# Kernel tuning notes

Measured on AMD Instinct MI355X. Metric: run time of the kernel, lower is better.

## Reference

```python
import jax, jax.numpy as jnp
import numpy as np

MLP_DIMS = [256, 128, 64, 32, 1]

def setup_inputs() -> dict:
    key = jax.random.key(0)
    ks = jax.random.split(key, 16)
    N, C, sp = 2, 256, 512
    inp = {
        'points': jax.random.normal(ks[0], (N, C, sp), dtype=jnp.float32),
        'heatMap': jax.random.uniform(ks[1], (N, sp, sp), dtype=jnp.float32),
        'mask': jnp.ones((N, sp, sp), dtype=jnp.float32),
        'positiveMask': jax.random.uniform(ks[2], (N, sp, sp), dtype=jnp.float32),
    }
    # MLP params: 256->128->64->32->1, Kaiming-ish scale
    for i, (din, dout) in enumerate(zip(MLP_DIMS[:-1], MLP_DIMS[1:])):
        inp[f'W{i}'] = jax.random.normal(ks[4 + i], (din, dout), dtype=jnp.float32) * (1.0 / np.sqrt(din))
        inp[f'b{i}'] = jnp.zeros((dout,), dtype=jnp.float32)
    return inp


def _mlp(x, Ws, bs):
    # Linear+ReLU cascade; final layer is a raw logit (no activation).
    n = len(Ws)
    for i, (W, b) in enumerate(zip(Ws, bs)):
        x = jnp.einsum('...i,io->...o', x, W) + b
        if i < n - 1:
            x = jax.nn.relu(x)
    return x


def _bce_with_logits(logits, targets):
    # stable elementwise BCE-with-logits, reduction='none'
    return jnp.maximum(logits, 0.0) - logits * targets + jnp.log1p(jnp.exp(-jnp.abs(logits)))


def reference(points, heatMap, mask, positiveMask, W0, b0, W1, b1, W2, b2, W3, b3):
    p = jnp.transpose(points, (0, 2, 1))          # (N, sp, C)
    X = p[:, :, None, :] + p[:, None, :, :]       # (N, sp, sp, C)
    pred = _mlp(X, [W0, W1, W2, W3], [b0, b1, b2, b3])[..., 0]  # (N, sp, sp)
    loss = _bce_with_logits(pred, heatMap) * mask * positiveMask
    loss = loss.sum() / positiveMask.sum()
    return (pred, loss)
```

## Files before the change

kernel.cpp:

```cpp
#include <hip/hip_runtime.h>
#include <stdint.h>

#define N_ 2
#define C_ 256
#define SP 512
#define H1 128
#define H2 64
#define H3 32
#define NTILE 1056
#define GRID 256

using f32x4 = __attribute__((ext_vector_type(4))) float;
using u32x4 = __attribute__((ext_vector_type(4))) unsigned int;
using s16x8 = __attribute__((ext_vector_type(8))) short;

__device__ __forceinline__ uint32_t f2bf_rne(float x) {
    uint32_t u = __builtin_bit_cast(uint32_t, x);
    return (u + 0x7FFFu + ((u >> 16) & 1u)) >> 16;
}
__device__ __forceinline__ float bf2f(uint32_t h) {
    return __builtin_bit_cast(float, h << 16);
}
__device__ __forceinline__ f32x4 ntload4(const float* p) {
    return __builtin_nontemporal_load((const f32x4*)p);
}

__device__ __forceinline__ void unrank_tile(int tau, int& n, int& iBase, int& jBase)
{
    int nn = (tau >= 528) ? 1 : 0;
    int u = tau - nn * 528;
    int bi = (int)((65.0f - sqrtf(4225.0f - 8.0f * (float)u)) * 0.5f);
    int s = bi * (65 - bi) / 2;
    while (s > u) { --bi; s = bi * (65 - bi) / 2; }
    while (u - s >= 32 - bi) { ++bi; s = bi * (65 - bi) / 2; }
    int bj = bi + (u - s);
    n = nn; iBase = bi * 16; jBase = bj * 16;
}

__global__ __launch_bounds__(512) void k_precompA(
    const float* __restrict__ points, const float* __restrict__ W0,
    const float* __restrict__ b0,
    const float* __restrict__ W1, const float* __restrict__ W2,
    float* __restrict__ A,
    short* __restrict__ W1Th, short* __restrict__ W2Th, short* __restrict__ W2Tl)
{
    int t = threadIdx.x;
    int k4 = t & 31;
    int team = t >> 5;
    int rloc = team & 3, cq = team >> 2;
    int row = blockIdx.x * 4 + rloc;
    int n = row >> 9, i = row & (SP - 1);
    const float* pb = points + (size_t)n * C_ * SP + i;
    f32x4 p0 = {0.f, 0.f, 0.f, 0.f}, p1 = {0.f, 0.f, 0.f, 0.f};
    int c0 = cq * 64;
#pragma unroll 8
    for (int c = c0; c < c0 + 64; c += 2) {
        float s0 = pb[(size_t)c * SP];
        float s1 = pb[(size_t)(c + 1) * SP];
        f32x4 w0v = *(const f32x4*)(W0 + c * H1 + k4 * 4);
        f32x4 w1v = *(const f32x4*)(W0 + (c + 1) * H1 + k4 * 4);
#pragma unroll
        for (int e = 0; e < 4; ++e) {
            p0[e] = fmaf(s0, w0v[e], p0[e]);
            p1[e] = fmaf(s1, w1v[e], p1[e]);
        }
    }
#pragma unroll
    for (int e = 0; e < 4; ++e) p0[e] += p1[e];
    __shared__ f32x4 part[16][32];
    part[team][k4] = p0;
    __syncthreads();
    int r2 = t >> 7, kk = t & 127;
    float s = 0.5f * b0[kk]
            + part[r2][kk >> 2][kk & 3] + part[r2 + 4][kk >> 2][kk & 3]
            + part[r2 + 8][kk >> 2][kk & 3] + part[r2 + 12][kk >> 2][kk & 3];
    A[(size_t)(blockIdx.x * 4 + r2) * H1 + kk] = s;

    int gid = blockIdx.x * 512 + t;
    int gstride = gridDim.x * 512;
    for (int idx = gid; idx < H2 * H1; idx += gstride) {
        int col = idx >> 7, k = idx & 127;
        int sidx = col * 128 + ((((k >> 3) ^ (col & 15)) << 3) | (k & 7));
        W1Th[sidx] = (short)f2bf_rne(W1[k * H2 + col]);
    }
    for (int idx = gid; idx < H3 * H2; idx += gstride) {
        int col = idx >> 6, k = idx & 63;
        float wv = W2[k * H3 + col];
        uint32_t h = f2bf_rne(wv);
        int sidx = col * 64 + ((((k >> 3) ^ (col & 7)) << 3) | (k & 7));
        W2Th[sidx] = (short)h;
        W2Tl[sidx] = (short)f2bf_rne(wv - bf2f(h));
    }
}

__global__ __launch_bounds__(512, 2) void k_main(
    const float* __restrict__ A,
    const short* __restrict__ wtab,
    const float* __restrict__ b1, const float* __restrict__ b2,
    const float* __restrict__ W3, const float* __restrict__ b3,
    const float* __restrict__ heat, const float* __restrict__ mask,
    const float* __restrict__ pos,
    float* __restrict__ pred, float* __restrict__ accum)
{
    __shared__ __align__(16) char smem[32768 + 16384 + 8192 + 2176 + 64];
    int t = threadIdx.x;
    int bid = blockIdx.x;
    int l = t & 63, w = t >> 6;
    int lc = l & 15, kg = l >> 4;
    char* x2 = smem + 32768 + w * 2048;
    char* x3 = smem + 32768 + 16384 + w * 1024;
    char* zbB = smem + 32768 + 16384 + 8192;
    float* rb = (float*)(smem + 32768 + 16384 + 8192 + 2176);

    const short* lw1h = wtab;
    const short* lw2h = wtab + 8192;
    const short* lw2l = wtab + 10240;

    int rST = t >> 5, segST = t & 31;

    s16x8 bw3;
    {
        f32x4 wa = *(const f32x4*)(W3 + kg * 8);
        f32x4 wb = *(const f32x4*)(W3 + kg * 8 + 4);
        u32x4 wp;
#pragma unroll
        for (int p = 0; p < 2; ++p) {
            wp[p]     = f2bf_rne(wa[2 * p]) | (f2bf_rne(wa[2 * p + 1]) << 16);
            wp[2 + p] = f2bf_rne(wb[2 * p]) | (f2bf_rne(wb[2 * p + 1]) << 16);
        }
        bw3 = __builtin_bit_cast(s16x8, wp);
    }
    float b3v = b3[0];

    float num = 0.0f, den = 0.0f;

    {
        int n0, ib0, jb0; unrank_tile(bid, n0, ib0, jb0);
        const float* Ab = A + (size_t)n0 * SP * H1;
        f32x4 va = ntload4(Ab + (size_t)(ib0 + rST) * H1 + segST * 4);
        f32x4 vb = ntload4(Ab + (size_t)(jb0 + rST) * H1 + segST * 4);
        *(f32x4*)(smem + rST * 512 + ((segST ^ rST) << 4)) = va;
        *(f32x4*)(smem + 8192 + rST * 512 + ((segST ^ rST) << 4)) = vb;
    }
    __syncthreads();

    int cur = 0, itp = 0;
    for (int tau = bid; tau < NTILE; tau += GRID, cur ^= 1, itp ^= 1) {
        int n, iBase, jBase; unrank_tile(tau, n, iBase, jBase);
        char* aiA = smem + cur * 16384;
        char* ajA = aiA + 8192;
        float* zb = (float*)(zbB + itp * 1088);

        bool hn = (tau + GRID < NTILE);
        f32x4 sva, svb;
        if (hn) {
            int n1, ib1, jb1; unrank_tile(tau + GRID, n1, ib1, jb1);
            const float* Ab1 = A + (size_t)n1 * SP * H1;
            sva = ntload4(Ab1 + (size_t)(ib1 + rST) * H1 + segST * 4);
            svb = ntload4(Ab1 + (size_t)(jb1 + rST) * H1 + segST * 4);
        }

        int pr = (t & 255) >> 4, pc = t & 15;
        size_t idx_e = (t < 256)
            ? ((size_t)n * SP + iBase + pr) * SP + (jBase + pc)
            : ((size_t)n * SP + jBase + pr) * SP + (iBase + pc);
        float tg_e = __builtin_nontemporal_load(heat + idx_e);
        float mk_e = __builtin_nontemporal_load(mask + idx_e);
        float pm_e = __builtin_nontemporal_load(pos + idx_e);

        f32x4 acc[2][4];
#pragma unroll
        for (int cf = 0; cf < 4; ++cf) {
            float bv = b1[cf * 16 + lc];
            acc[0][cf] = (f32x4){bv, bv, bv, bv};
            acc[1][cf] = (f32x4){bv, bv, bv, bv};
        }
#pragma unroll
        for (int ks = 0; ks < 4; ++ks) {
            int g0 = ks * 8 + kg * 2;
            f32x4 aj0 = *(const f32x4*)(ajA + lc * 512 + ((g0 ^ lc) << 4));
            f32x4 aj1 = *(const f32x4*)(ajA + lc * 512 + (((g0 + 1) ^ lc) << 4));
#pragma unroll
            for (int m = 0; m < 2; ++m) {
                int rl = 2 * w + m;
                f32x4 ai0 = *(const f32x4*)(aiA + rl * 512 + ((g0 ^ rl) << 4));
                f32x4 ai1 = *(const f32x4*)(aiA + rl * 512 + (((g0 + 1) ^ rl) << 4));
                float xs[8];
#pragma unroll
                for (int e = 0; e < 4; ++e) {
                    xs[e]     = fmaxf(ai0[e] + aj0[e], 0.0f);
                    xs[4 + e] = fmaxf(ai1[e] + aj1[e], 0.0f);
                }
                u32x4 hw;
#pragma unroll
                for (int p = 0; p < 4; ++p)
                    hw[p] = f2bf_rne(xs[2 * p]) | (f2bf_rne(xs[2 * p + 1]) << 16);
                s16x8 ahi = __builtin_bit_cast(s16x8, hw);
#pragma unroll
                for (int cf = 0; cf < 4; ++cf) {
                    int boff = (cf * 16 + lc) * 128 + (((ks * 4 + kg) ^ lc) << 3);
                    s16x8 bhi = *(const s16x8*)(lw1h + boff);
                    acc[m][cf] = __builtin_amdgcn_mfma_f32_16x16x32_bf16(ahi, bhi, acc[m][cf], 0, 0, 0);
                }
            }
        }

#pragma unroll
        for (int m = 0; m < 2; ++m) {
#pragma unroll
            for (int cf = 0; cf < 4; ++cf) {
                int g = cf * 2 + (lc >> 3);
#pragma unroll
                for (int r = 0; r < 4; ++r) {
                    int row = kg * 4 + r;
                    int off = row * 128 + ((g ^ (row & 7)) << 4) + (lc & 7) * 2;
                    *(short*)(x2 + off) = (short)f2bf_rne(fmaxf(acc[m][cf][r], 0.0f));
                }
            }
            f32x4 acc2[2];
#pragma unroll
            for (int cf = 0; cf < 2; ++cf) {
                float bv = b2[cf * 16 + lc];
                acc2[cf] = (f32x4){bv, bv, bv, bv};
            }
#pragma unroll
            for (int ks = 0; ks < 2; ++ks) {
                int aoff = lc * 128 + (((ks * 4 + kg) ^ (lc & 7)) << 4);
                s16x8 xa = *(const s16x8*)(x2 + aoff);
#pragma unroll
                for (int cf = 0; cf < 2; ++cf) {
                    int b2off = (cf * 16 + lc) * 64 + (((ks * 4 + kg) ^ (lc & 7)) << 3);
                    s16x8 bh = *(const s16x8*)(lw2h + b2off);
                    s16x8 bl = *(const s16x8*)(lw2l + b2off);
                    acc2[cf] = __builtin_amdgcn_mfma_f32_16x16x32_bf16(xa, bh, acc2[cf], 0, 0, 0);
                    acc2[cf] = __builtin_amdgcn_mfma_f32_16x16x32_bf16(xa, bl, acc2[cf], 0, 0, 0);
                }
            }
#pragma unroll
            for (int cf = 0; cf < 2; ++cf) {
                int g = cf * 2 + (lc >> 3);
#pragma unroll
                for (int r = 0; r < 4; ++r) {
                    int row = kg * 4 + r;
                    int off = row * 64 + ((g ^ (row & 3)) << 4) + (lc & 7) * 2;
                    *(short*)(x3 + off) = (short)f2bf_rne(fmaxf(acc2[cf][r], 0.0f));
                }
            }
            int a4off = lc * 64 + ((kg ^ (lc & 3)) << 4);
            s16x8 x4 = *(const s16x8*)(x3 + a4off);
            f32x4 acc3 = (f32x4){b3v, b3v, b3v, b3v};
            acc3 = __builtin_amdgcn_mfma_f32_16x16x32_bf16(x4, bw3, acc3, 0, 0, 0);
            if (lc == 0) {
#pragma unroll
                for (int r = 0; r < 4; ++r)
                    zb[(2 * w + m) * 17 + kg * 4 + r] = acc3[r];
            }
        }

        if (hn) {
            char* Aalt = smem + (cur ^ 1) * 16384;
            *(f32x4*)(Aalt + rST * 512 + ((segST ^ rST) << 4)) = sva;
            *(f32x4*)(Aalt + 8192 + rST * 512 + ((segST ^ rST) << 4)) = svb;
        }
        __syncthreads();

        if (t < 256) {
            int i = iBase + pr, j = jBase + pc;
            if (j >= i) {
                float z = zb[pr * 17 + pc];
                __builtin_nontemporal_store(z, pred + idx_e);
                float bce = fmaxf(z, 0.0f) - z * tg_e + __logf(1.0f + __expf(-fabsf(z)));
                num += bce * mk_e * pm_e;
                den += pm_e;
            }
        } else {
            int J = jBase + pr, I = iBase + pc;
            if (J > I) {
                float z = zb[pc * 17 + pr];
                __builtin_nontemporal_store(z, pred + idx_e);
                float bce = fmaxf(z, 0.0f) - z * tg_e + __logf(1.0f + __expf(-fabsf(z)));
                num += bce * mk_e * pm_e;
                den += pm_e;
            }
        }
    }

#pragma unroll
    for (int off = 32; off > 0; off >>= 1) {
        num += __shfl_down(num, off, 64);
        den += __shfl_down(den, off, 64);
    }
    if (l == 0) { rb[w] = num; rb[8 + w] = den; }
    __syncthreads();
    if (t == 0) {
        float sn = 0.0f, sd = 0.0f;
#pragma unroll
        for (int q = 0; q < 8; ++q) { sn += rb[q]; sd += rb[8 + q]; }
        atomicAdd(&accum[0], sn);
        atomicAdd(&accum[1], sd);
    }
}

__global__ void k_final(const float* __restrict__ accum, float* __restrict__ out)
{
    out[0] = accum[0] / accum[1];
}

extern "C" void kernel_launch(void* const* d_in, const int* in_sizes, int n_in,
                              void* d_out, int out_size, void* d_ws, size_t ws_size,
                              hipStream_t stream)
{
    const float* points = (const float*)d_in[0];
    const float* heat   = (const float*)d_in[1];
    const float* mask   = (const float*)d_in[2];
    const float* pos    = (const float*)d_in[3];
    const float* W0     = (const float*)d_in[4];
    const float* b0     = (const float*)d_in[5];
    const float* W1     = (const float*)d_in[6];
    const float* b1     = (const float*)d_in[7];
    const float* W2     = (const float*)d_in[8];
    const float* b2     = (const float*)d_in[9];
    const float* W3     = (const float*)d_in[10];
    const float* b3     = (const float*)d_in[11];

    float* pred = (float*)d_out;
    float* loss = pred + (size_t)N_ * SP * SP;

    char* ws = (char*)d_ws;
    float* accum = (float*)ws;
    float* A     = (float*)(ws + 256);
    short* W1Th  = (short*)(ws + 256 + 524288);
    short* W2Th  = (short*)(ws + 256 + 524288 + 16384);
    short* W2Tl  = (short*)(ws + 256 + 524288 + 20480);

    hipMemsetAsync(d_ws, 0, 256, stream);
    k_precompA<<<256, 512, 0, stream>>>(points, W0, b0, W1, W2, A, W1Th, W2Th, W2Tl);
    k_main<<<GRID, 512, 0, stream>>>(
        A, W1Th, b1, b2, W3, b3, heat, mask, pos, pred, accum);
    k_final<<<1, 1, 0, stream>>>(accum, loss);
}
```

Before: 43.46 us.

## Replace final MFMA layer with fp32 shuffle reduction and batch layer-2 across row blocks

Layer 3 (32->1) no longer goes through a bf16 LDS staging buffer and an MFMA. It is now computed in fp32 as a per-lane dot with W3 followed by a 16-lane xor-shuffle reduction. Layer 2 is restructured to write both m-halves to LDS first and then issue all MFMAs together, which gives more independent MFMA chains. The grid size is also doubled from 256 to 512 blocks. This adds shuffle instructions and per-wave LDS while removing the x3 buffer and an LDS round trip, and the larger grid changes how tiles are spread across CUs.

```diff
diff --git a/kernel.cpp b/kernel.cpp
--- a/kernel.cpp
+++ b/kernel.cpp
@@ -8,7 +8,7 @@
 #define H2 64
 #define H3 32
 #define NTILE 1056
-#define GRID 256
+#define GRID 512
 
 using f32x4 = __attribute__((ext_vector_type(4))) float;
 using u32x4 = __attribute__((ext_vector_type(4))) unsigned int;
@@ -102,15 +102,14 @@
     const float* __restrict__ pos,
     float* __restrict__ pred, float* __restrict__ accum)
 {
-    __shared__ __align__(16) char smem[32768 + 16384 + 8192 + 2176 + 64];
+    __shared__ __align__(16) char smem[32768 + 32768 + 2176 + 64];
     int t = threadIdx.x;
     int bid = blockIdx.x;
     int l = t & 63, w = t >> 6;
     int lc = l & 15, kg = l >> 4;
-    char* x2 = smem + 32768 + w * 2048;
-    char* x3 = smem + 32768 + 16384 + w * 1024;
-    char* zbB = smem + 32768 + 16384 + 8192;
-    float* rb = (float*)(smem + 32768 + 16384 + 8192 + 2176);
+    char* x2b = smem + 32768 + w * 4096;
+    char* zbB = smem + 32768 + 32768;
+    float* rb = (float*)(smem + 32768 + 32768 + 2176);
 
     const short* lw1h = wtab;
     const short* lw2h = wtab + 8192;
@@ -118,18 +117,7 @@
 
     int rST = t >> 5, segST = t & 31;
 
-    s16x8 bw3;
-    {
-        f32x4 wa = *(const f32x4*)(W3 + kg * 8);
-        f32x4 wb = *(const f32x4*)(W3 + kg * 8 + 4);
-        u32x4 wp;
-#pragma unroll
-        for (int p = 0; p < 2; ++p) {
-            wp[p]     = f2bf_rne(wa[2 * p]) | (f2bf_rne(wa[2 * p + 1]) << 16);
-            wp[2 + p] = f2bf_rne(wb[2 * p]) | (f2bf_rne(wb[2 * p + 1]) << 16);
-        }
-        bw3 = __builtin_bit_cast(s16x8, wp);
-    }
+    float w3a = W3[lc], w3b = W3[16 + lc];
     float b3v = b3[0];
 
     float num = 0.0f, den = 0.0f;
@@ -207,6 +195,7 @@
 
 #pragma unroll
         for (int m = 0; m < 2; ++m) {
+            char* x2 = x2b + m * 2048;
 #pragma unroll
             for (int cf = 0; cf < 4; ++cf) {
                 int g = cf * 2 + (lc >> 3);
@@ -217,44 +206,53 @@
                     *(short*)(x2 + off) = (short)f2bf_rne(fmaxf(acc[m][cf][r], 0.0f));
                 }
             }
-            f32x4 acc2[2];
-#pragma unroll
-            for (int cf = 0; cf < 2; ++cf) {
-                float bv = b2[cf * 16 + lc];
-                acc2[cf] = (f32x4){bv, bv, bv, bv};
-            }
-#pragma unroll
-            for (int ks = 0; ks < 2; ++ks) {
+        }
+        f32x4 acc2[2][2];
+#pragma unroll
+        for (int cf = 0; cf < 2; ++cf) {
+            float bv = b2[cf * 16 + lc];
+            acc2[0][cf] = (f32x4){bv, bv, bv, bv};
+            acc2[1][cf] = (f32x4){bv, bv, bv, bv};
+        }
+#pragma unroll
+        for (int ks = 0; ks < 2; ++ks) {
+#pragma unroll
+            for (int m = 0; m < 2; ++m) {
                 int aoff = lc * 128 + (((ks * 4 + kg) ^ (lc & 7)) << 4);
-                s16x8 xa = *(const s16x8*)(x2 + aoff);
+                s16x8 xa = *(const s16x8*)(x2b + m * 2048 + aoff);
 #pragma unroll
                 for (int cf = 0; cf < 2; ++cf) {
                     int b2off = (cf * 16 + lc) * 64 + (((ks * 4 + kg) ^ (lc & 7)) << 3);
                     s16x8 bh = *(const s16x8*)(lw2h + b2off);
                     s16x8 bl = *(const s16x8*)(lw2l + b2off);
-                    acc2[cf] = __builtin_amdgcn_mfma_f32_16x16x32_bf16(xa, bh, acc2[cf], 0, 0, 0);
-                    acc2[cf] = __builtin_amdgcn_mfma_f32_16x16x32_bf16(xa, bl, acc2[cf], 0, 0, 0);
+                    acc2[m][cf] = __builtin_amdgcn_mfma_f32_16x16x32_bf16(xa, bh, acc2[m][cf], 0, 0, 0);
+                    acc2[m][cf] = __builtin_amdgcn_mfma_f32_16x16x32_bf16(xa, bl, acc2[m][cf], 0, 0, 0);
                 }
             }
-#pragma unroll
-            for (int cf = 0; cf < 2; ++cf) {
-                int g = cf * 2 + (lc >> 3);
-#pragma unroll
-                for (int r = 0; r < 4; ++r) {
-                    int row = kg * 4 + r;
-                    int off = row * 64 + ((g ^ (row & 3)) << 4) + (lc & 7) * 2;
-                    *(short*)(x3 + off) = (short)f2bf_rne(fmaxf(acc2[cf][r], 0.0f));
-                }
-            }
-            int a4off = lc * 64 + ((kg ^ (lc & 3)) << 4);
-            s16x8 x4 = *(const s16x8*)(x3 + a4off);
-            f32x4 acc3 = (f32x4){b3v, b3v, b3v, b3v};
-            acc3 = __builtin_amdgcn_mfma_f32_16x16x32_bf16(x4, bw3, acc3, 0, 0, 0);
-            if (lc == 0) {
+        }
+        float zr[2][4];
+#pragma unroll
+        for (int m = 0; m < 2; ++m)
+#pragma unroll
+            for (int r = 0; r < 4; ++r)
+                zr[m][r] = fmaxf(acc2[m][0][r], 0.0f) * w3a
+                         + fmaxf(acc2[m][1][r], 0.0f) * w3b;
+#pragma unroll
+        for (int off = 1; off < 16; off <<= 1) {
+#pragma unroll
+            for (int m = 0; m < 2; ++m)
 #pragma unroll
                 for (int r = 0; r < 4; ++r)
-                    zb[(2 * w + m) * 17 + kg * 4 + r] = acc3[r];
-            }
+                    zr[m][r] += __shfl_xor(zr[m][r], off, 64);
+        }
+#pragma unroll
+        for (int m = 0; m < 2; ++m) {
+            float zsel = zr[m][0];
+            zsel = (lc == 1) ? zr[m][1] : zsel;
+            zsel = (lc == 2) ? zr[m][2] : zsel;
+            zsel = (lc == 3) ? zr[m][3] : zsel;
+            if (lc < 4)
+                zb[(2 * w + m) * 17 + kg * 4 + lc] = zsel + b3v;
         }
 
         if (hn) {
```

New measurement: 49.55 us. 14.0% more time.
